# Kernel optimization log

Hardware: AMD Instinct MI355X
Metric: run time of the kernel (lower is better)

Reference implementation:

```python
import jax, jax.numpy as jnp
import numpy as np
import math

B, T, C = 4, 2048, 1024
H = 16
D = C // H  # head dim = 64


def setup_inputs() -> dict:
    key = jax.random.key(0)
    k1, k2, k3 = jax.random.split(key, 3)
    x = jax.random.normal(k1, (B, T, C), dtype=jnp.float32)
    # torch nn.Linear weight layout: [out_features, in_features]
    w_attn = jax.random.normal(k2, (3 * C, C), dtype=jnp.float32) * (1.0 / math.sqrt(C))
    w_proj = jax.random.normal(k3, (C, C), dtype=jnp.float32) * (1.0 / math.sqrt(C))
    return {"x": x, "w_attn": w_attn, "w_proj": w_proj}


def reference(x, w_attn, w_proj):
    b, t, c = x.shape
    # qkv projection: Linear(C, 3C) with no bias -> x @ w_attn.T
    qkv = jnp.einsum('btc,oc->bto', x, w_attn)  # [B,T,3C]
    q, k, v = jnp.split(qkv, 3, axis=-1)
    # [B,T,C] -> [B,H,T,D]
    q = q.reshape(b, t, H, D).transpose(0, 2, 1, 3)
    k = k.reshape(b, t, H, D).transpose(0, 2, 1, 3)
    v = v.reshape(b, t, H, D).transpose(0, 2, 1, 3)
    scale = 1.0 / math.sqrt(D)
    att = jnp.einsum('bhqd,bhkd->bhqk', q, k) * scale  # [B,H,T,T]
    # NOTE: faithful to source — the naive branch applies NO causal mask
    att = jax.nn.softmax(att, axis=-1)
    y = jnp.einsum('bhqk,bhkd->bhqd', att, v)  # [B,H,T,D]
    y = y.transpose(0, 2, 1, 3).reshape(b, t, c)
    return jnp.einsum('btc,oc->bto', y, w_proj)
```

## Files before the change

kernel.cpp:

```cpp
#include <hip/hip_runtime.h>

#define T_SEQ 2048
#define C_DIM 1024
#define H_NUM 16
#define H_D   64
#define B_NUM 4
#define M_ROWS 8192

typedef __attribute__((ext_vector_type(4))) float f32x4;
typedef __attribute__((ext_vector_type(8))) short bf16x8;

__device__ __forceinline__ unsigned short f2bf(float f) {
  union { float f; unsigned int u; } a;
  a.f = f;
  unsigned int u = a.u;
  u += 0x7fffu + ((u >> 16) & 1u);
  return (unsigned short)(u >> 16);
}

__device__ __forceinline__ unsigned int fbits(float f) {
  union { float f; unsigned int u; } a; a.f = f; return a.u;
}

__device__ __forceinline__ unsigned int pack_hi(float a, float b) {
#if __has_builtin(__builtin_amdgcn_perm)
  return __builtin_amdgcn_perm(fbits(b), fbits(a), 0x07060302u);
#else
  return (fbits(b) & 0xffff0000u) | (fbits(a) >> 16);
#endif
}

__device__ __forceinline__ void gload_lds16(const unsigned short* g, unsigned short* l) {
  __builtin_amdgcn_global_load_lds(
      (const __attribute__((address_space(1))) unsigned int*)g,
      (__attribute__((address_space(3))) unsigned int*)l, 16, 0, 0);
}

__global__ __launch_bounds__(256) void cast_all_kernel(const float* __restrict__ x,
                                                       const float* __restrict__ wa,
                                                       const float* __restrict__ wp,
                                                       unsigned short* __restrict__ xb,
                                                       unsigned short* __restrict__ wab,
                                                       unsigned short* __restrict__ wpb) {
  int i = blockIdx.x * 256 + threadIdx.x;
  const float* src;
  unsigned short* dst;
  int off;
  if (i < 2097152) {
    src = x; dst = xb; off = i;
  } else if (i < 2883584) {
    src = wa; dst = wab; off = i - 2097152;
  } else {
    src = wp; dst = wpb; off = i - 2883584;
  }
  float4 v = reinterpret_cast<const float4*>(src)[off];
  ushort4 o;
  o.x = f2bf(v.x); o.y = f2bf(v.y); o.z = f2bf(v.z); o.w = f2bf(v.w);
  reinterpret_cast<ushort4*>(dst)[off] = o;
}

__global__ __launch_bounds__(512, 4) void gemm_qkv_kernel(
    const unsigned short* __restrict__ A,
    const unsigned short* __restrict__ Bw,
    unsigned short* __restrict__ q_ws,
    unsigned short* __restrict__ k_ws,
    unsigned short* __restrict__ v_ws) {
  constexpr int KK = 1024;
  constexpr int KT = KK / 64;

  __shared__ unsigned short lds[16384 + 12288];

  const int bid = blockIdx.x;
  const int logical = (bid & 7) * 64 + (bid >> 3);
  const int rb = logical >> 4, cb = logical & 15;

  const int t = threadIdx.x;
  const int w = t >> 6, l = t & 63;
  const int wr = w >> 2, wc = w & 3;
  const int lq = l & 15, lg = l >> 4;

  const size_t a_base = (size_t)(rb * 256) * KK;
  const size_t b_base = (size_t)(cb * 192) * KK;

  int aRow[4], aGs[4];
#pragma unroll
  for (int i = 0; i < 4; ++i) {
    int c = t + 512 * i;
    aRow[i] = c >> 3;
    aGs[i] = (c & 7) ^ (aRow[i] & 7);
  }
  int bRow[3], bGs[3];
#pragma unroll
  for (int i = 0; i < 3; ++i) {
    int c = t + 512 * i;
    bRow[i] = c >> 3;
    bGs[i] = (c & 7) ^ (bRow[i] & 7);
  }

  f32x4 acc[8][3] = {};

  for (int kt = 0; kt < KT; ++kt) {
    const int ko = kt * 64;
#pragma unroll
    for (int i = 0; i < 4; ++i)
      gload_lds16(A + a_base + (size_t)aRow[i] * KK + ko + aGs[i] * 8,
                  &lds[(t + 512 * i) * 8]);
#pragma unroll
    for (int i = 0; i < 3; ++i)
      gload_lds16(Bw + b_base + (size_t)bRow[i] * KK + ko + bGs[i] * 8,
                  &lds[16384 + (t + 512 * i) * 8]);
    __syncthreads();

#pragma unroll
    for (int kk = 0; kk < 2; ++kk) {
      const int sg = kk * 4 + lg;
      bf16x8 bfv[3];
#pragma unroll
      for (int j = 0; j < 3; ++j) {
        int R = wc * 48 + j * 16 + lq;
        bfv[j] = *reinterpret_cast<const bf16x8*>(&lds[16384 + (R * 8 + (sg ^ (R & 7))) * 8]);
      }
#pragma unroll
      for (int mq = 0; mq < 2; ++mq) {
        bf16x8 af[4];
#pragma unroll
        for (int i = 0; i < 4; ++i) {
          int R = wr * 128 + mq * 64 + i * 16 + lq;
          af[i] = *reinterpret_cast<const bf16x8*>(&lds[(R * 8 + (sg ^ (R & 7))) * 8]);
        }
#pragma unroll
        for (int i = 0; i < 4; ++i)
#pragma unroll
          for (int j = 0; j < 3; ++j)
            acc[mq * 4 + i][j] =
                __builtin_amdgcn_mfma_f32_16x16x32_bf16(af[i], bfv[j], acc[mq * 4 + i][j], 0, 0, 0);
      }
    }
    __syncthreads();
  }

#pragma unroll
  for (int f = 0; f < 8; ++f) {
#pragma unroll
    for (int j = 0; j < 3; ++j) {
#pragma unroll
      for (int r = 0; r < 4; ++r) {
        int m = rb * 256 + wr * 128 + f * 16 + lg * 4 + r;
        int n = cb * 192 + wc * 48 + j * 16 + lq;
        float v = acc[f][j][r];
        int which = n >> 10;
        int h = (n >> 6) & 15;
        int d = n & 63;
        int b = m >> 11;
        int tt = m & 2047;
        int bh = b * H_NUM + h;
        if (which == 0) {
          q_ws[((size_t)bh * T_SEQ + tt) * H_D + d] = f2bf(v * 0.18033688f);
        } else if (which == 1) {
          k_ws[((size_t)bh * T_SEQ + tt) * H_D + d] = f2bf(v);
        } else {
          int k0 = tt & 63;
          int tp = (tt & ~63) | ((k0 & 12) << 1) | ((k0 & 48) >> 3) | (k0 & 1) | ((k0 & 2) << 4);
          v_ws[((size_t)bh * H_D + d) * T_SEQ + tp] = f2bf(v);
        }
      }
    }
  }
}

__global__ __launch_bounds__(256, 4) void gemm_proj_kernel(
    const unsigned short* __restrict__ A,
    const unsigned short* __restrict__ Bw,
    float* __restrict__ outf) {
  constexpr int KK = 1024;
  constexpr int KT = KK / 64;

  __shared__ unsigned short lds[16384];

  const int bid = blockIdx.x;
  const int logical = (bid & 7) * 64 + (bid >> 3);
  const int rb = logical >> 3, cb = logical & 7;

  const int t = threadIdx.x;
  const int w = t >> 6, l = t & 63;
  const int wr = w >> 1, wc = w & 1;
  const int lq = l & 15, lg = l >> 4;

  const size_t a_base = (size_t)(rb * 128) * KK;
  const size_t b_base = (size_t)(cb * 128) * KK;

  int s_row[4], s_gs[4];
#pragma unroll
  for (int i = 0; i < 4; ++i) {
    int c = t + 256 * i;
    s_row[i] = c >> 3;
    s_gs[i] = (c & 7) ^ (s_row[i] & 7);
  }

  f32x4 acc[4][4] = {};

  for (int kt = 0; kt < KT; ++kt) {
    const int ko = kt * 64;
#pragma unroll
    for (int i = 0; i < 4; ++i) {
      unsigned short* la = &lds[(t + 256 * i) * 8];
      gload_lds16(A + a_base + (size_t)s_row[i] * KK + ko + s_gs[i] * 8, la);
      gload_lds16(Bw + b_base + (size_t)s_row[i] * KK + ko + s_gs[i] * 8, la + 8192);
    }
    __syncthreads();

#pragma unroll
    for (int kk = 0; kk < 2; ++kk) {
      const int sg = kk * 4 + lg;
      bf16x8 af[4], bfv[4];
#pragma unroll
      for (int i = 0; i < 4; ++i) {
        int R = wr * 64 + i * 16 + lq;
        af[i] = *reinterpret_cast<const bf16x8*>(&lds[(R * 8 + (sg ^ (R & 7))) * 8]);
      }
#pragma unroll
      for (int j = 0; j < 4; ++j) {
        int R = wc * 64 + j * 16 + lq;
        bfv[j] = *reinterpret_cast<const bf16x8*>(&lds[8192 + (R * 8 + (sg ^ (R & 7))) * 8]);
      }
#pragma unroll
      for (int i = 0; i < 4; ++i)
#pragma unroll
        for (int j = 0; j < 4; ++j)
          acc[i][j] = __builtin_amdgcn_mfma_f32_16x16x32_bf16(af[i], bfv[j], acc[i][j], 0, 0, 0);
    }
    __syncthreads();
  }

#pragma unroll
  for (int i = 0; i < 4; ++i)
#pragma unroll
    for (int j = 0; j < 4; ++j)
#pragma unroll
      for (int r = 0; r < 4; ++r) {
        int m = rb * 128 + wr * 64 + i * 16 + lg * 4 + r;
        int n = cb * 128 + wc * 64 + j * 16 + lq;
        outf[(size_t)m * 1024 + n] = acc[i][j][r];
      }
}

__global__ __launch_bounds__(256, 2) void attn_kernel(
    const unsigned short* __restrict__ qw,
    const unsigned short* __restrict__ kw,
    const unsigned short* __restrict__ vtw,
    unsigned short* __restrict__ yw) {
  __shared__ unsigned short kv_lds[3][8192];

  const int bid = blockIdx.x;
  const int bh = (bid & 7) * 8 + ((bid >> 3) & 7);
  const int qblk = bid >> 6;

  const int t = threadIdx.x;
  const int w = t >> 6, l = t & 63;
  const int lq = l & 15, lg = l >> 4;
  const int qbase = qblk * 256 + w * 64;
  const size_t head_off = (size_t)bh * T_SEQ * H_D;

  bf16x8 aq[4][2];
#pragma unroll
  for (int qg = 0; qg < 4; ++qg)
#pragma unroll
    for (int kk = 0; kk < 2; ++kk)
      aq[qg][kk] = *reinterpret_cast<const bf16x8*>(
          qw + head_off + (size_t)(qbase + qg * 16 + lq) * H_D + kk * 32 + lg * 8);

  const unsigned short* sbase[4];
  int sstep[4];
#pragma unroll
  for (int i = 0; i < 4; ++i) {
    int c = w * 64 + l + 256 * i;
    if (c < 512) {
      int row = c >> 3, sl = (c & 7) ^ (row & 7);
      sbase[i] = kw + head_off + row * H_D + sl * 8;
      sstep[i] = 64 * H_D;
    } else {
      int c2 = c - 512;
      int row = c2 >> 3, sl = (c2 & 7) ^ (row & 7);
      sbase[i] = vtw + head_off + (size_t)row * T_SEQ + sl * 8;
      sstep[i] = 64;
    }
  }

  unsigned short* bA = &kv_lds[0][0];
  unsigned short* bB = &kv_lds[1][0];
  unsigned short* bC = &kv_lds[2][0];

#define STAGE(KV, DST)                                                              \
  { _Pragma("unroll")                                                               \
    for (int i = 0; i < 4; ++i)                                                     \
      gload_lds16(sbase[i] + (size_t)(KV) * sstep[i], (DST) + (w * 64 + 256 * i) * 8); }

  STAGE(0, bA)
  STAGE(1, bB)

  f32x4 y[4][4] = {};
  float lrow[4] = {0.f, 0.f, 0.f, 0.f};
  union pa_t { bf16x8 v; unsigned int u[4]; };

  for (int kv = 0; kv < T_SEQ / 64; ++kv) {
    if (kv == T_SEQ / 64 - 1) {
      asm volatile("s_waitcnt vmcnt(0)" ::: "memory");
    } else {
      asm volatile("s_waitcnt vmcnt(4)" ::: "memory");
    }
    __builtin_amdgcn_s_barrier();

    bf16x8 kf[8], vf[8];
#pragma unroll
    for (int f = 0; f < 8; ++f) {
      int row = (f >> 1) * 16 + lq;
      int sl = ((f & 1) * 4 + lg) ^ (lq & 7);
      kf[f] = *reinterpret_cast<const bf16x8*>(bA + row * 64 + sl * 8);
    }
#pragma unroll
    for (int db = 0; db < 4; ++db)
#pragma unroll
      for (int ks = 0; ks < 2; ++ks) {
        int row = db * 16 + lq;
        int sl = (ks * 4 + lg) ^ (lq & 7);
        vf[db * 2 + ks] = *reinterpret_cast<const bf16x8*>(bA + 4096 + row * 64 + sl * 8);
      }

    pa_t pa0[4], pa1[4];
#pragma unroll
    for (int qg = 0; qg < 4; ++qg) {
      f32x4 s[4];
#pragma unroll
      for (int tt = 0; tt < 4; ++tt) {
        f32x4 z = {0.f, 0.f, 0.f, 0.f};
        s[tt] = __builtin_amdgcn_mfma_f32_16x16x32_bf16(kf[tt * 2], aq[qg][0], z, 0, 0, 0);
        s[tt] = __builtin_amdgcn_mfma_f32_16x16x32_bf16(kf[tt * 2 + 1], aq[qg][1], s[tt], 0, 0, 0);
      }
      float acc_e = 0.f;
#pragma unroll
      for (int tt = 0; tt < 4; ++tt) {
        float e0 = __builtin_amdgcn_exp2f(s[tt][0]);
        float e1 = __builtin_amdgcn_exp2f(s[tt][1]);
        float e2 = __builtin_amdgcn_exp2f(s[tt][2]);
        float e3 = __builtin_amdgcn_exp2f(s[tt][3]);
        pa0[qg].u[tt] = pack_hi(e0, e1);
        pa1[qg].u[tt] = pack_hi(e2, e3);
        acc_e += (e0 + e1) + (e2 + e3);
      }
      lrow[qg] += acc_e;
    }

#pragma unroll
    for (int qg = 0; qg < 4; ++qg)
#pragma unroll
      for (int db = 0; db < 4; ++db) {
        y[qg][db] = __builtin_amdgcn_mfma_f32_16x16x32_bf16(pa0[qg].v, vf[db * 2], y[qg][db], 0, 0, 0);
        y[qg][db] = __builtin_amdgcn_mfma_f32_16x16x32_bf16(pa1[qg].v, vf[db * 2 + 1], y[qg][db], 0, 0, 0);
      }

    if (kv + 2 < T_SEQ / 64) STAGE(kv + 2, bC)

    unsigned short* tmp = bA; bA = bB; bB = bC; bC = tmp;
  }
#undef STAGE

  const int b = bh >> 4, h = bh & 15;
#pragma unroll
  for (int qg = 0; qg < 4; ++qg) {
    float sm = lrow[qg];
    sm += __shfl_xor(sm, 16);
    sm += __shfl_xor(sm, 32);
    float inv = 1.0f / sm;
#pragma unroll
    for (int r = 0; r < 4; ++r) {
      float iv = __shfl(inv, lg * 4 + r);
      int row = qbase + qg * 16 + lg * 4 + r;
#pragma unroll
      for (int db = 0; db < 4; ++db) {
        int d = db * 16 + lq;
        yw[((size_t)(b * T_SEQ + row)) * C_DIM + h * 64 + d] = f2bf(y[qg][db][r] * iv);
      }
    }
  }
}

extern "C" void kernel_launch(void* const* d_in, const int* in_sizes, int n_in,
                              void* d_out, int out_size, void* d_ws, size_t ws_size,
                              hipStream_t stream) {
  (void)in_sizes; (void)n_in; (void)out_size; (void)ws_size;
  const float* x      = (const float*)d_in[0];
  const float* w_attn = (const float*)d_in[1];
  const float* w_proj = (const float*)d_in[2];
  float* out = (float*)d_out;

  unsigned short* ws = (unsigned short*)d_ws;
  const size_t XB = (size_t)M_ROWS * C_DIM;
  unsigned short* xb  = ws;
  unsigned short* wab = xb + XB;
  unsigned short* wpb = wab + (size_t)3072 * 1024;
  unsigned short* qws = wpb + (size_t)1024 * 1024;
  unsigned short* kws = qws + XB;
  unsigned short* vws = kws + XB;
  unsigned short* yws = xb;

  cast_all_kernel<<<3145728 / 256, 256, 0, stream>>>(x, w_attn, w_proj, xb, wab, wpb);

  gemm_qkv_kernel<<<512, 512, 0, stream>>>(xb, wab, qws, kws, vws);
  attn_kernel<<<512, 256, 0, stream>>>(qws, kws, vws, yws);
  gemm_proj_kernel<<<512, 256, 0, stream>>>(yws, wpb, out);
}
```

Baseline: 190.8 us.

## Double-buffer QKV GEMM LDS with k-split staging and interleaved prefetch phases

The QKV projection GEMM moves from a single LDS buffer, loaded fully and then synchronised each k-tile, to a double-buffered scheme. Each 64-wide k-tile is split into two 32-wide halves with a new swizzled layout, and the prefetch of later halves is interleaved between MFMA phases using explicit barriers, vmcnt waits and setprio. The aim is to hide global-to-LDS latency behind matrix math. In exchange it doubles LDS use, lowers the occupancy hint from 4 to 2, and relies on hand-counted vmcnt waits that must match the load counts exactly.

```diff
diff --git a/kernel.cpp b/kernel.cpp
--- a/kernel.cpp
+++ b/kernel.cpp
@@ -59,7 +59,7 @@
   reinterpret_cast<ushort4*>(dst)[off] = o;
 }
 
-__global__ __launch_bounds__(512, 4) void gemm_qkv_kernel(
+__global__ __launch_bounds__(512, 2) void gemm_qkv8_kernel(
     const unsigned short* __restrict__ A,
     const unsigned short* __restrict__ Bw,
     unsigned short* __restrict__ q_ws,
@@ -68,7 +68,7 @@
   constexpr int KK = 1024;
   constexpr int KT = KK / 64;
 
-  __shared__ unsigned short lds[16384 + 12288];
+  __shared__ __align__(16) unsigned short lds[2][28672];
 
   const int bid = blockIdx.x;
   const int logical = (bid & 7) * 64 + (bid >> 3);
@@ -82,62 +82,97 @@
   const size_t a_base = (size_t)(rb * 256) * KK;
   const size_t b_base = (size_t)(cb * 192) * KK;
 
-  int aRow[4], aGs[4];
-#pragma unroll
-  for (int i = 0; i < 4; ++i) {
+  const unsigned short* aSrc[2];
+  int aOffL[2];
+#pragma unroll
+  for (int i = 0; i < 2; ++i) {
     int c = t + 512 * i;
-    aRow[i] = c >> 3;
-    aGs[i] = (c & 7) ^ (aRow[i] & 7);
-  }
-  int bRow[3], bGs[3];
-#pragma unroll
-  for (int i = 0; i < 3; ++i) {
+    int p = c >> 3, sp = (c & 7) ^ (p & 7);
+    int r = (p << 1) | (sp >> 2);
+    aSrc[i] = A + a_base + (size_t)r * KK + (sp & 3) * 8;
+    aOffL[i] = c * 8;
+  }
+  const unsigned short* bSrc[2];
+  int bOffL[2];
+#pragma unroll
+  for (int i = 0; i < 2; ++i) {
     int c = t + 512 * i;
-    bRow[i] = c >> 3;
-    bGs[i] = (c & 7) ^ (bRow[i] & 7);
+    int cc = (c < 768) ? c : 0;
+    int p = cc >> 3, sp = (cc & 7) ^ (p & 7);
+    int r = (p << 1) | (sp >> 2);
+    bSrc[i] = Bw + b_base + (size_t)r * KK + (sp & 3) * 8;
+    bOffL[i] = cc * 8;
+  }
+
+#define STAGE_A(KT_, KS)                                                      \
+  { unsigned short* d_ = &lds[(KT_) & 1][(KS) * 8192];                        \
+    _Pragma("unroll")                                                         \
+    for (int i_ = 0; i_ < 2; ++i_)                                            \
+      gload_lds16(aSrc[i_] + (KT_) * 64 + (KS) * 32, d_ + aOffL[i_]); }
+
+#define STAGE_B(KT_, KS)                                                      \
+  { unsigned short* d_ = &lds[(KT_) & 1][16384 + (KS) * 6144];                \
+    gload_lds16(bSrc[0] + (KT_) * 64 + (KS) * 32, d_ + bOffL[0]);             \
+    if (t < 256)                                                              \
+      gload_lds16(bSrc[1] + (KT_) * 64 + (KS) * 32, d_ + bOffL[1]); }
+
+  int aRd[2][4], bRd[3];
+#pragma unroll
+  for (int ch = 0; ch < 2; ++ch)
+#pragma unroll
+    for (int i = 0; i < 4; ++i) {
+      int R = wr * 128 + ch * 64 + i * 16 + lq;
+      int p = R >> 1;
+      int s8 = ((((R & 1) << 2) | lg)) ^ (p & 7);
+      aRd[ch][i] = p * 64 + s8 * 8;
+    }
+#pragma unroll
+  for (int j = 0; j < 3; ++j) {
+    int R = wc * 48 + j * 16 + lq;
+    int p = R >> 1;
+    int s8 = ((((R & 1) << 2) | lg)) ^ (p & 7);
+    bRd[j] = p * 64 + s8 * 8;
   }
 
   f32x4 acc[8][3] = {};
 
+#define PHASE(KT_, KS, CH, STAGE_STMT, VM_STMT)                               \
+  { const unsigned short* buf_ = &lds[(KT_) & 1][0];                          \
+    bf16x8 af[4], bfv[3];                                                     \
+    _Pragma("unroll")                                                         \
+    for (int i_ = 0; i_ < 4; ++i_)                                            \
+      af[i_] = *reinterpret_cast<const bf16x8*>(buf_ + (KS) * 8192 + aRd[CH][i_]); \
+    _Pragma("unroll")                                                         \
+    for (int j_ = 0; j_ < 3; ++j_)                                            \
+      bfv[j_] = *reinterpret_cast<const bf16x8*>(buf_ + 16384 + (KS) * 6144 + bRd[j_]); \
+    STAGE_STMT;                                                               \
+    __builtin_amdgcn_s_barrier();                                             \
+    __builtin_amdgcn_s_setprio(1);                                            \
+    _Pragma("unroll")                                                         \
+    for (int i_ = 0; i_ < 4; ++i_)                                            \
+      _Pragma("unroll")                                                       \
+      for (int j_ = 0; j_ < 3; ++j_)                                          \
+        acc[(CH) * 4 + i_][j_] = __builtin_amdgcn_mfma_f32_16x16x32_bf16(     \
+            af[i_], bfv[j_], acc[(CH) * 4 + i_][j_], 0, 0, 0);                \
+    __builtin_amdgcn_s_setprio(0);                                            \
+    VM_STMT;                                                                  \
+    __builtin_amdgcn_s_barrier(); }
+
+  STAGE_A(0, 0) STAGE_B(0, 0) STAGE_A(0, 1) STAGE_B(0, 1) STAGE_A(1, 0) STAGE_B(1, 0)
+  asm volatile("s_waitcnt vmcnt(3)" ::: "memory");
+  __builtin_amdgcn_s_barrier();
+
   for (int kt = 0; kt < KT; ++kt) {
-    const int ko = kt * 64;
-#pragma unroll
-    for (int i = 0; i < 4; ++i)
-      gload_lds16(A + a_base + (size_t)aRow[i] * KK + ko + aGs[i] * 8,
-                  &lds[(t + 512 * i) * 8]);
-#pragma unroll
-    for (int i = 0; i < 3; ++i)
-      gload_lds16(Bw + b_base + (size_t)bRow[i] * KK + ko + bGs[i] * 8,
-                  &lds[16384 + (t + 512 * i) * 8]);
-    __syncthreads();
-
-#pragma unroll
-    for (int kk = 0; kk < 2; ++kk) {
-      const int sg = kk * 4 + lg;
-      bf16x8 bfv[3];
-#pragma unroll
-      for (int j = 0; j < 3; ++j) {
-        int R = wc * 48 + j * 16 + lq;
-        bfv[j] = *reinterpret_cast<const bf16x8*>(&lds[16384 + (R * 8 + (sg ^ (R & 7))) * 8]);
-      }
-#pragma unroll
-      for (int mq = 0; mq < 2; ++mq) {
-        bf16x8 af[4];
-#pragma unroll
-        for (int i = 0; i < 4; ++i) {
-          int R = wr * 128 + mq * 64 + i * 16 + lq;
-          af[i] = *reinterpret_cast<const bf16x8*>(&lds[(R * 8 + (sg ^ (R & 7))) * 8]);
-        }
-#pragma unroll
-        for (int i = 0; i < 4; ++i)
-#pragma unroll
-          for (int j = 0; j < 3; ++j)
-            acc[mq * 4 + i][j] =
-                __builtin_amdgcn_mfma_f32_16x16x32_bf16(af[i], bfv[j], acc[mq * 4 + i][j], 0, 0, 0);
-      }
-    }
-    __syncthreads();
-  }
+    PHASE(kt, 0, 0, { if (kt + 1 < KT) STAGE_A(kt + 1, 1) }, {})
+    PHASE(kt, 0, 1, { if (kt + 1 < KT) STAGE_B(kt + 1, 1) }, {})
+    PHASE(kt, 1, 0, { if (kt + 2 < KT) STAGE_A(kt + 2, 0) }, {})
+    PHASE(kt, 1, 1, { if (kt + 2 < KT) STAGE_B(kt + 2, 0) },
+          { if (kt < KT - 2) { asm volatile("s_waitcnt vmcnt(3)" ::: "memory"); }
+            else if (kt == KT - 2) { asm volatile("s_waitcnt vmcnt(0)" ::: "memory"); } })
+  }
+#undef PHASE
+#undef STAGE_A
+#undef STAGE_B
 
 #pragma unroll
   for (int f = 0; f < 8; ++f) {
@@ -405,7 +440,7 @@
 
   cast_all_kernel<<<3145728 / 256, 256, 0, stream>>>(x, w_attn, w_proj, xb, wab, wpb);
 
-  gemm_qkv_kernel<<<512, 512, 0, stream>>>(xb, wab, qws, kws, vws);
+  gemm_qkv8_kernel<<<512, 512, 0, stream>>>(xb, wab, qws, kws, vws);
   attn_kernel<<<512, 256, 0, stream>>>(qws, kws, vws, yws);
   gemm_proj_kernel<<<512, 256, 0, stream>>>(yws, wpb, out);
 }
```

Result: no change. 189.4 us (-0.7%).

## Double-buffer QKV GEMM LDS with interleaved prefetch and phased MFMA scheduling

Applied to the files above, without the earlier changes.

Rewrites the QKV projection GEMM main loop to double-buffer LDS, so the next K-tile's global-to-LDS loads are issued in pieces between four MFMA phases instead of load-then-compute with full syncthreads. The A tile is relaid out as two 32-column halves with a new swizzle. Fine-grained vmcnt waits, raw barriers and setprio are used to overlap memory with compute. This doubles LDS use and lowers the occupancy hint to 2, and it relies on the hand-tuned waitcnt counts being correct.

```diff
diff --git a/kernel.cpp b/kernel.cpp
--- a/kernel.cpp
+++ b/kernel.cpp
@@ -59,7 +59,7 @@
   reinterpret_cast<ushort4*>(dst)[off] = o;
 }
 
-__global__ __launch_bounds__(512, 4) void gemm_qkv_kernel(
+__global__ __launch_bounds__(512, 2) void gemm_qkv8_kernel(
     const unsigned short* __restrict__ A,
     const unsigned short* __restrict__ Bw,
     unsigned short* __restrict__ q_ws,
@@ -68,7 +68,7 @@
   constexpr int KK = 1024;
   constexpr int KT = KK / 64;
 
-  __shared__ unsigned short lds[16384 + 12288];
+  __shared__ __align__(16) unsigned short lds[2][28672];
 
   const int bid = blockIdx.x;
   const int logical = (bid & 7) * 64 + (bid >> 3);
@@ -82,62 +82,140 @@
   const size_t a_base = (size_t)(rb * 256) * KK;
   const size_t b_base = (size_t)(cb * 192) * KK;
 
-  int aRow[4], aGs[4];
-#pragma unroll
-  for (int i = 0; i < 4; ++i) {
+  const unsigned short* aSrc[2];
+  int aOffL[2];
+#pragma unroll
+  for (int i = 0; i < 2; ++i) {
     int c = t + 512 * i;
-    aRow[i] = c >> 3;
-    aGs[i] = (c & 7) ^ (aRow[i] & 7);
-  }
-  int bRow[3], bGs[3];
+    int p = c >> 3, sp = (c & 7) ^ (p & 7);
+    int r = (p << 1) | (sp >> 2);
+    aSrc[i] = A + a_base + (size_t)r * KK + (sp & 3) * 8;
+    aOffL[i] = c * 8;
+  }
+  const unsigned short* bSrc[3];
+  int bOffL[3];
 #pragma unroll
   for (int i = 0; i < 3; ++i) {
     int c = t + 512 * i;
-    bRow[i] = c >> 3;
-    bGs[i] = (c & 7) ^ (bRow[i] & 7);
-  }
+    int r = c >> 3, s = (c & 7) ^ (r & 7);
+    bSrc[i] = Bw + b_base + (size_t)r * KK + s * 8;
+    bOffL[i] = c * 8;
+  }
+
+#define STAGE_A(KT_, KS)                                                      \
+  { unsigned short* d_ = &lds[(KT_) & 1][(KS) * 8192];                        \
+    _Pragma("unroll")                                                         \
+    for (int i_ = 0; i_ < 2; ++i_)                                            \
+      gload_lds16(aSrc[i_] + (KT_) * 64 + (KS) * 32, d_ + aOffL[i_]); }
+
+#define STAGE_B(KT_)                                                          \
+  { unsigned short* d_ = &lds[(KT_) & 1][16384];                              \
+    _Pragma("unroll")                                                         \
+    for (int i_ = 0; i_ < 3; ++i_)                                            \
+      gload_lds16(bSrc[i_] + (KT_) * 64, d_ + bOffL[i_]); }
+
+  int aRd[2][4];
+#pragma unroll
+  for (int mq = 0; mq < 2; ++mq)
+#pragma unroll
+    for (int i = 0; i < 4; ++i) {
+      int R = wr * 128 + mq * 64 + i * 16 + lq;
+      int p = R >> 1;
+      int s8 = ((((R & 1) << 2) | lg)) ^ (p & 7);
+      aRd[mq][i] = p * 64 + s8 * 8;
+    }
+  int bRd[2][3];
+#pragma unroll
+  for (int kk = 0; kk < 2; ++kk)
+#pragma unroll
+    for (int j = 0; j < 3; ++j) {
+      int R = wc * 48 + j * 16 + lq;
+      int sg = kk * 4 + lg;
+      bRd[kk][j] = R * 64 + (sg ^ (R & 7)) * 8;
+    }
 
   f32x4 acc[8][3] = {};
+  bf16x8 bfv[3];
+
+#define MM(MQ)                                                                \
+  { _Pragma("unroll")                                                         \
+    for (int i_ = 0; i_ < 4; ++i_)                                            \
+      _Pragma("unroll")                                                       \
+      for (int j_ = 0; j_ < 3; ++j_)                                          \
+        acc[(MQ) * 4 + i_][j_] = __builtin_amdgcn_mfma_f32_16x16x32_bf16(     \
+            af[i_], bfv[j_], acc[(MQ) * 4 + i_][j_], 0, 0, 0); }
+
+#define BAR()  __builtin_amdgcn_s_barrier()
+#define LG0()  asm volatile("s_waitcnt lgkmcnt(0)" ::: "memory")
+
+  STAGE_B(0) STAGE_A(0, 0) STAGE_A(0, 1)
+  asm volatile("s_waitcnt vmcnt(2)" ::: "memory");
+  BAR();
 
   for (int kt = 0; kt < KT; ++kt) {
-    const int ko = kt * 64;
-#pragma unroll
-    for (int i = 0; i < 4; ++i)
-      gload_lds16(A + a_base + (size_t)aRow[i] * KK + ko + aGs[i] * 8,
-                  &lds[(t + 512 * i) * 8]);
-#pragma unroll
-    for (int i = 0; i < 3; ++i)
-      gload_lds16(Bw + b_base + (size_t)bRow[i] * KK + ko + bGs[i] * 8,
-                  &lds[16384 + (t + 512 * i) * 8]);
-    __syncthreads();
-
-#pragma unroll
-    for (int kk = 0; kk < 2; ++kk) {
-      const int sg = kk * 4 + lg;
-      bf16x8 bfv[3];
-#pragma unroll
-      for (int j = 0; j < 3; ++j) {
-        int R = wc * 48 + j * 16 + lq;
-        bfv[j] = *reinterpret_cast<const bf16x8*>(&lds[16384 + (R * 8 + (sg ^ (R & 7))) * 8]);
-      }
-#pragma unroll
-      for (int mq = 0; mq < 2; ++mq) {
-        bf16x8 af[4];
-#pragma unroll
-        for (int i = 0; i < 4; ++i) {
-          int R = wr * 128 + mq * 64 + i * 16 + lq;
-          af[i] = *reinterpret_cast<const bf16x8*>(&lds[(R * 8 + (sg ^ (R & 7))) * 8]);
-        }
-#pragma unroll
-        for (int i = 0; i < 4; ++i)
-#pragma unroll
-          for (int j = 0; j < 3; ++j)
-            acc[mq * 4 + i][j] =
-                __builtin_amdgcn_mfma_f32_16x16x32_bf16(af[i], bfv[j], acc[mq * 4 + i][j], 0, 0, 0);
-      }
-    }
-    __syncthreads();
-  }
+    const unsigned short* buf = &lds[kt & 1][0];
+    {
+      bf16x8 af[4];
+#pragma unroll
+      for (int i = 0; i < 4; ++i)
+        af[i] = *reinterpret_cast<const bf16x8*>(buf + aRd[0][i]);
+#pragma unroll
+      for (int j = 0; j < 3; ++j)
+        bfv[j] = *reinterpret_cast<const bf16x8*>(buf + 16384 + bRd[0][j]);
+      if (kt + 1 < KT) STAGE_B(kt + 1)
+      BAR(); LG0();
+      __builtin_amdgcn_s_setprio(1);
+      MM(0)
+      __builtin_amdgcn_s_setprio(0);
+      BAR();
+    }
+    {
+      bf16x8 af[4];
+#pragma unroll
+      for (int i = 0; i < 4; ++i)
+        af[i] = *reinterpret_cast<const bf16x8*>(buf + aRd[1][i]);
+      if (kt + 1 < KT) STAGE_A(kt + 1, 0)
+      BAR(); LG0();
+      __builtin_amdgcn_s_setprio(1);
+      MM(1)
+      __builtin_amdgcn_s_setprio(0);
+      if (kt < KT - 1) { asm volatile("s_waitcnt vmcnt(5)" ::: "memory"); }
+      else            { asm volatile("s_waitcnt vmcnt(0)" ::: "memory"); }
+      BAR();
+    }
+    {
+      bf16x8 af[4];
+#pragma unroll
+      for (int i = 0; i < 4; ++i)
+        af[i] = *reinterpret_cast<const bf16x8*>(buf + 8192 + aRd[0][i]);
+#pragma unroll
+      for (int j = 0; j < 3; ++j)
+        bfv[j] = *reinterpret_cast<const bf16x8*>(buf + 16384 + bRd[1][j]);
+      if (kt + 1 < KT) STAGE_A(kt + 1, 1)
+      BAR(); LG0();
+      __builtin_amdgcn_s_setprio(1);
+      MM(0)
+      __builtin_amdgcn_s_setprio(0);
+      BAR();
+    }
+    {
+      bf16x8 af[4];
+#pragma unroll
+      for (int i = 0; i < 4; ++i)
+        af[i] = *reinterpret_cast<const bf16x8*>(buf + 8192 + aRd[1][i]);
+      BAR(); LG0();
+      __builtin_amdgcn_s_setprio(1);
+      MM(1)
+      __builtin_amdgcn_s_setprio(0);
+      if (kt < KT - 1) { asm volatile("s_waitcnt vmcnt(2)" ::: "memory"); }
+      BAR();
+    }
+  }
+#undef MM
+#undef BAR
+#undef LG0
+#undef STAGE_A
+#undef STAGE_B
 
 #pragma unroll
   for (int f = 0; f < 8; ++f) {
@@ -405,7 +483,7 @@
 
   cast_all_kernel<<<3145728 / 256, 256, 0, stream>>>(x, w_attn, w_proj, xb, wab, wpb);
 
-  gemm_qkv_kernel<<<512, 512, 0, stream>>>(xb, wab, qws, kws, vws);
+  gemm_qkv8_kernel<<<512, 512, 0, stream>>>(xb, wab, qws, kws, vws);
   attn_kernel<<<512, 256, 0, stream>>>(qws, kws, vws, yws);
   gemm_proj_kernel<<<512, 256, 0, stream>>>(yws, wpb, out);
 }
```

Result: faster. 187.0 us (-2.0%).
